# Performance work log

Measured on AMD Instinct MI355X. Metric: run time of the kernel, lower is better.

Reference implementation:

```python
import jax, jax.numpy as jnp
import numpy as np

N = 50000
E = 800000
D = 512
H = 256
K = 16
COLLAPSE_REG = 1.0


def setup_inputs() -> dict:
    key = jax.random.key(0)
    ks = jax.random.split(key, 8)
    embeddings = jax.random.normal(ks[0], (N, D), dtype=jnp.float32)
    edge_src = jax.random.randint(ks[1], (E,), 0, N, dtype=jnp.int32)
    edge_dst = jax.random.randint(ks[2], (E,), 0, N, dtype=jnp.int32)
    # GCNConv params (glorot-ish scaling)
    W1 = jax.random.normal(ks[3], (D, H), dtype=jnp.float32) / np.sqrt(D)
    b1 = jnp.zeros((H,), dtype=jnp.float32)
    W2 = jax.random.normal(ks[4], (H, H), dtype=jnp.float32) / np.sqrt(H)
    b2 = jnp.zeros((H,), dtype=jnp.float32)
    Wa = jax.random.normal(ks[5], (H, K), dtype=jnp.float32) / np.sqrt(H)
    ba = jnp.zeros((K,), dtype=jnp.float32)
    return {"embeddings": embeddings, "edge_src": edge_src, "edge_dst": edge_dst,
            "W1": W1, "b1": b1, "W2": W2, "b2": b2, "Wa": Wa, "ba": ba}


def _gcn_conv(x, W, b, src, dst, dis):
    # PyG GCNConv: transform then D^{-1/2}(A+I)D^{-1/2} aggregation + bias.
    x = x @ W                                   # [N, out]
    norm = dis[src] * dis[dst]                  # [E]
    agg = jax.ops.segment_sum(x[src] * norm[:, None], dst, num_segments=N)
    agg = agg + (dis * dis)[:, None] * x        # self-loop term
    return agg + b


def reference(embeddings, edge_src, edge_dst, W1, b1, W2, b2, Wa, ba):
    # symmetric-norm degrees with self-loops (edge weight 1)
    deg = 1.0 + jax.ops.segment_sum(jnp.ones((E,), jnp.float32), edge_dst, num_segments=N)
    dis = jax.lax.rsqrt(deg)                    # deg > 0 always (self-loop)

    x = jax.nn.selu(_gcn_conv(embeddings, W1, b1, edge_src, edge_dst, dis))
    x_skip = x  # dropout is identity in eval
    x = jax.nn.selu(_gcn_conv(x, W2, b2, edge_src, edge_dst, dis))
    x = x + x_skip
    assignments = jax.nn.softmax(x @ Wa + ba, axis=1)   # [N, K]

    # ---- DMoN losses (faithful to original, incl. scalar normalizer) ----
    degrees = jax.ops.segment_sum(jnp.ones((E,), jnp.float32), edge_src, num_segments=N)  # row sums of A
    m = degrees.sum() / 2.0
    AS = jax.ops.segment_sum(assignments[edge_dst], edge_src, num_segments=N)  # A @ S, [N, K]
    trace_pooled = jnp.sum(assignments * AS)    # trace(S^T A S)
    dS = degrees @ assignments                  # [K]
    normalizer = jnp.dot(dS, dS) / (2.0 * m)    # scalar (as in original code)
    spectral_loss = -(trace_pooled - K * normalizer) / (2.0 * m)

    cluster_sizes = assignments.sum(axis=0)     # [K]
    collapse_loss = jnp.linalg.norm(cluster_sizes) / N * jnp.sqrt(jnp.float32(K)) - 1.0
    entropy = -jnp.sum(assignments * jnp.log(assignments + 1e-8)) / N
    entropy_loss = -0.1 * entropy
    total_loss = spectral_loss + COLLAPSE_REG * collapse_loss + entropy_loss

    pooled = (assignments / (cluster_sizes + 1e-8)).T @ embeddings  # [K, D]
    return (assignments, pooled, spectral_loss, COLLAPSE_REG * collapse_loss, total_loss, entropy_loss)
```

## Files before the change

kernel.cpp:

```cpp
#include <hip/hip_runtime.h>
#include <hip/hip_fp16.h>
#include <math.h>

#define NN 50000
#define EE 800000
#define DD 512
#define HH 256
#define KK 16
#define NB_SCAN 196

typedef _Float16 half8_t __attribute__((ext_vector_type(8)));
typedef float f32x4 __attribute__((ext_vector_type(4)));

__global__ void zero_kernel(int* __restrict__ p, int n) {
    int i = blockIdx.x * blockDim.x + threadIdx.x;
    if (i < n) p[i] = 0;
}

__global__ void count_kernel(const int4* __restrict__ src4, const int4* __restrict__ dst4,
                             int* __restrict__ indeg, int* __restrict__ outdeg) {
    int e = blockIdx.x * blockDim.x + threadIdx.x;
    if (e < EE / 4) {
        int4 s = src4[e], d = dst4[e];
        atomicAdd(&outdeg[s.x], 1); atomicAdd(&outdeg[s.y], 1);
        atomicAdd(&outdeg[s.z], 1); atomicAdd(&outdeg[s.w], 1);
        atomicAdd(&indeg[d.x], 1);  atomicAdd(&indeg[d.y], 1);
        atomicAdd(&indeg[d.z], 1);  atomicAdd(&indeg[d.w], 1);
    }
}

__global__ void scan_p1(const int* __restrict__ in, int* __restrict__ part, int n,
                        const int* __restrict__ outdeg, float* __restrict__ dis,
                        float* __restrict__ degf) {
    __shared__ int tile[256];
    int t = threadIdx.x;
    int i = blockIdx.x * 256 + t;
    int v = (i < n) ? in[i] : 0;
    tile[t] = v;
    if (i < n) {
        dis[i]  = 1.0f / sqrtf(1.0f + (float)v);
        degf[i] = (float)outdeg[i];
    }
    __syncthreads();
    for (int o = 128; o > 0; o >>= 1) {
        if (t < o) tile[t] += tile[t + o];
        __syncthreads();
    }
    if (t == 0) part[blockIdx.x] = tile[0];
}

__global__ void scan_p2(int* __restrict__ part, int nb, int* __restrict__ off_end) {
    __shared__ int tile[256];
    int t = threadIdx.x;
    int v = (t < nb) ? part[t] : 0;
    tile[t] = v;
    __syncthreads();
    for (int o = 1; o < 256; o <<= 1) {
        int x = (t >= o) ? tile[t - o] : 0;
        __syncthreads();
        tile[t] += x;
        __syncthreads();
    }
    if (t < nb) part[t] = tile[t] - v;
    if (t == 255) *off_end = tile[255];
}

__global__ void scan_p3(const int* __restrict__ in, const int* __restrict__ part,
                        int* __restrict__ out, int n) {
    __shared__ int tile[256];
    int t = threadIdx.x;
    int i = blockIdx.x * 256 + t;
    int v = (i < n) ? in[i] : 0;
    tile[t] = v;
    __syncthreads();
    for (int o = 1; o < 256; o <<= 1) {
        int x = (t >= o) ? tile[t - o] : 0;
        __syncthreads();
        tile[t] += x;
        __syncthreads();
    }
    if (i < n) out[i] = part[blockIdx.x] + tile[t] - v;
}

__global__ void transpose_w(const float* __restrict__ W1, __half* __restrict__ Wt1,
                            const float* __restrict__ W2, __half* __restrict__ Wt2,
                            const float* __restrict__ Wa, __half* __restrict__ WaT) {
    int i = blockIdx.x * 256 + threadIdx.x;
    if (i < DD * HH) {
        int k = i / HH, n = i % HH;
        Wt1[(size_t)n * DD + k] = __float2half(W1[i]);
    } else if (i < DD * HH + HH * HH) {
        int j = i - DD * HH;
        int k = j / HH, n = j % HH;
        Wt2[(size_t)n * HH + k] = __float2half(W2[j]);
    } else if (i < DD * HH + HH * HH + HH * KK) {
        int j = i - DD * HH - HH * HH;
        int k = j / KK, n = j % KK;
        WaT[n * HH + k] = __float2half(Wa[j]);
    }
}

__global__ __launch_bounds__(256) void gemm1_scatter(
        const float* __restrict__ A, const __half* __restrict__ Bt,
        __half* __restrict__ C, int M,
        const int4* __restrict__ src4, const int4* __restrict__ dst4,
        const int* __restrict__ off, int* __restrict__ cur, int* __restrict__ nbr) {
    constexpr int SROW = 36;
    constexpr int EPG  = 4;
    constexpr int GPR  = 8;
    constexpr int RPP  = 32;
    constexpr int NP   = 4;
    constexpr int KI   = DD / 32;

    __shared__ float As[2][128 * SROW];

    int b = blockIdx.x;
    int t = threadIdx.x;
    if (b >= 784) {
        int e = (b - 784) * 256 + t;
        if (e < EE / 4) {
            int4 s = src4[e], d = dst4[e];
            int p;
            p = atomicAdd(&cur[d.x], 1); nbr[off[d.x] + p] = s.x;
            p = atomicAdd(&cur[d.y], 1); nbr[off[d.y] + p] = s.y;
            p = atomicAdd(&cur[d.z], 1); nbr[off[d.z] + p] = s.z;
            p = atomicAdd(&cur[d.w], 1); nbr[off[d.w] + p] = s.w;
        }
        return;
    }

    int wave = t >> 6, lane = t & 63, quad = lane >> 4, l16 = lane & 15;
    int row0 = (b >> 1) * 128, col0 = (b & 1) * 128;
    int wm = (wave & 1) * 64, wn = (wave >> 1) * 64;
    int srow = t / GPR, sg = t % GPR;

    f32x4 acc[4][4] = {};
    uint4 sreg[NP];
    uint4 bcur[4];

    const __half* brow[4];
#pragma unroll
    for (int ni = 0; ni < 4; ni++)
        brow[ni] = Bt + (size_t)(col0 + wn + ni * 16 + l16) * DD + quad * 8;

    auto gloadA = [&](int k0) {
#pragma unroll
        for (int p = 0; p < NP; p++) {
            int gr = row0 + p * RPP + srow;
            if (gr < M)
                sreg[p] = *(const uint4*)(A + (size_t)gr * DD + k0 + sg * EPG);
            else
                sreg[p] = make_uint4(0, 0, 0, 0);
        }
    };
    auto sstore = [&](int buf) {
#pragma unroll
        for (int p = 0; p < NP; p++)
            *(uint4*)&As[buf][(p * RPP + srow) * SROW + sg * EPG] = sreg[p];
    };

    gloadA(0);
#pragma unroll
    for (int ni = 0; ni < 4; ni++) bcur[ni] = *(const uint4*)(brow[ni]);
    sstore(0);
    __syncthreads();

#pragma unroll
    for (int i = 0; i < KI; i++) {
        int cur_b = i & 1;
        uint4 bnext[4];
        if (i + 1 < KI) {
            gloadA((i + 1) * 32);
#pragma unroll
            for (int ni = 0; ni < 4; ni++)
                bnext[ni] = *(const uint4*)(brow[ni] + (i + 1) * 32);
        }

        half8_t af[4];
#pragma unroll
        for (int mi = 0; mi < 4; mi++) {
            int row = wm + mi * 16 + l16;
            const float* pl = &As[cur_b][0] + row * SROW + quad * 8;
            float4 x0 = *(const float4*)pl;
            float4 x1 = *(const float4*)(pl + 4);
            half8_t h;
            h[0] = (_Float16)x0.x; h[1] = (_Float16)x0.y;
            h[2] = (_Float16)x0.z; h[3] = (_Float16)x0.w;
            h[4] = (_Float16)x1.x; h[5] = (_Float16)x1.y;
            h[6] = (_Float16)x1.z; h[7] = (_Float16)x1.w;
            af[mi] = h;
        }
#pragma unroll
        for (int mi = 0; mi < 4; mi++)
#pragma unroll
            for (int ni = 0; ni < 4; ni++)
                acc[mi][ni] = __builtin_amdgcn_mfma_f32_16x16x32_f16(
                    af[mi], *(half8_t*)&bcur[ni], acc[mi][ni], 0, 0, 0);

        if (i + 1 < KI) {
            sstore(cur_b ^ 1);
#pragma unroll
            for (int ni = 0; ni < 4; ni++) bcur[ni] = bnext[ni];
        }
        __syncthreads();
    }

#pragma unroll
    for (int mi = 0; mi < 4; mi++) {
#pragma unroll
        for (int r = 0; r < 4; r++) {
            int rr = row0 + wm + mi * 16 + quad * 4 + r;
            if (rr < M) {
#pragma unroll
                for (int ni = 0; ni < 4; ni++) {
                    C[(size_t)rr * HH + col0 + wn + ni * 16 + l16] =
                        __float2half(acc[mi][ni][r]);
                }
            }
        }
    }
}

template <typename TA, int KDIM>
__global__ __launch_bounds__(256) void mfma_gemm(const TA* __restrict__ A,
                                                 const __half* __restrict__ Bt,
                                                 __half* __restrict__ C, int M) {
    constexpr bool F32 = sizeof(TA) == 4;
    constexpr int SROW = F32 ? 36 : 40;
    constexpr int EPG  = F32 ? 4 : 8;
    constexpr int GPR  = 32 / EPG;
    constexpr int RPP  = 256 / GPR;
    constexpr int NP   = 128 / RPP;
    constexpr int KI   = KDIM / 32;

    __shared__ TA As[2][128 * SROW];

    int t = threadIdx.x;
    int wave = t >> 6, lane = t & 63, quad = lane >> 4, l16 = lane & 15;
    int row0 = blockIdx.x * 128, col0 = blockIdx.y * 128;
    int wm = (wave & 1) * 64, wn = (wave >> 1) * 64;
    int srow = t / GPR, sg = t % GPR;

    f32x4 acc[4][4] = {};
    uint4 sreg[NP];
    uint4 bcur[4];

    const __half* brow[4];
#pragma unroll
    for (int ni = 0; ni < 4; ni++)
        brow[ni] = Bt + (size_t)(col0 + wn + ni * 16 + l16) * KDIM + quad * 8;

    auto gloadA = [&](int k0) {
#pragma unroll
        for (int p = 0; p < NP; p++) {
            int gr = row0 + p * RPP + srow;
            if (gr < M)
                sreg[p] = *(const uint4*)(A + (size_t)gr * KDIM + k0 + sg * EPG);
            else
                sreg[p] = make_uint4(0, 0, 0, 0);
        }
    };
    auto sstore = [&](int buf) {
#pragma unroll
        for (int p = 0; p < NP; p++)
            *(uint4*)&As[buf][(p * RPP + srow) * SROW + sg * EPG] = sreg[p];
    };

    gloadA(0);
#pragma unroll
    for (int ni = 0; ni < 4; ni++) bcur[ni] = *(const uint4*)(brow[ni]);
    sstore(0);
    __syncthreads();

#pragma unroll
    for (int i = 0; i < KI; i++) {
        int cur = i & 1;
        uint4 bnext[4];
        if (i + 1 < KI) {
            gloadA((i + 1) * 32);
#pragma unroll
            for (int ni = 0; ni < 4; ni++)
                bnext[ni] = *(const uint4*)(brow[ni] + (i + 1) * 32);
        }

        half8_t af[4];
#pragma unroll
        for (int mi = 0; mi < 4; mi++) {
            int row = wm + mi * 16 + l16;
            if constexpr (F32) {
                const float* pl = (const float*)&As[cur][0] + row * SROW + quad * 8;
                float4 x0 = *(const float4*)pl;
                float4 x1 = *(const float4*)(pl + 4);
                half8_t h;
                h[0] = (_Float16)x0.x; h[1] = (_Float16)x0.y;
                h[2] = (_Float16)x0.z; h[3] = (_Float16)x0.w;
                h[4] = (_Float16)x1.x; h[5] = (_Float16)x1.y;
                h[6] = (_Float16)x1.z; h[7] = (_Float16)x1.w;
                af[mi] = h;
            } else {
                af[mi] = *(const half8_t*)&As[cur][row * SROW + quad * 8];
            }
        }
#pragma unroll
        for (int mi = 0; mi < 4; mi++)
#pragma unroll
            for (int ni = 0; ni < 4; ni++)
                acc[mi][ni] = __builtin_amdgcn_mfma_f32_16x16x32_f16(
                    af[mi], *(half8_t*)&bcur[ni], acc[mi][ni], 0, 0, 0);

        if (i + 1 < KI) {
            sstore(cur ^ 1);
#pragma unroll
            for (int ni = 0; ni < 4; ni++) bcur[ni] = bnext[ni];
        }
        __syncthreads();
    }

#pragma unroll
    for (int mi = 0; mi < 4; mi++) {
#pragma unroll
        for (int r = 0; r < 4; r++) {
            int rr = row0 + wm + mi * 16 + quad * 4 + r;
            if (rr < M) {
#pragma unroll
                for (int ni = 0; ni < 4; ni++) {
                    C[(size_t)rr * HH + col0 + wn + ni * 16 + l16] =
                        __float2half(acc[mi][ni][r]);
                }
            }
        }
    }
}

__device__ inline void fma8(float* acc, uint4 raw, float w) {
    const __half2* h = (const __half2*)&raw;
#pragma unroll
    for (int i = 0; i < 4; i++) {
        float2 f = __half22float2(h[i]);
        acc[2 * i]     += w * f.x;
        acc[2 * i + 1] += w * f.y;
    }
}

__global__ __launch_bounds__(256) void agg_selu(const __half* __restrict__ T,
                                                const float* __restrict__ dis,
                                                const int* __restrict__ off,
                                                const int* __restrict__ nbr,
                                                const float* __restrict__ bias,
                                                const __half* skip, __half* out) {
    int t = threadIdx.x;
    int l32 = t & 31;
    int n = blockIdx.x * 8 + (t >> 5);
    int c = l32 * 8;
    float dn = dis[n];

    float acc[8];
#pragma unroll
    for (int i = 0; i < 8; i++) acc[i] = 0.f;
    fma8(acc, *(const uint4*)(T + (size_t)n * HH + c), dn * dn);

    int s0 = off[n], s1 = off[n + 1];
    for (int base = s0; base < s1; base += 32) {
        int cnt = min(32, s1 - base);
        int sidv = 0; float sdsv = 0.f;
        if (l32 < cnt) {
            sidv = nbr[base + l32];
            sdsv = dis[sidv] * dn;
        }
        int j = 0;
        for (; j + 8 <= cnt; j += 8) {
            int a0 = __shfl(sidv, j, 32),     a1 = __shfl(sidv, j + 1, 32);
            int a2 = __shfl(sidv, j + 2, 32), a3 = __shfl(sidv, j + 3, 32);
            int a4 = __shfl(sidv, j + 4, 32), a5 = __shfl(sidv, j + 5, 32);
            int a6 = __shfl(sidv, j + 6, 32), a7 = __shfl(sidv, j + 7, 32);
            float w0 = __shfl(sdsv, j, 32),     w1 = __shfl(sdsv, j + 1, 32);
            float w2 = __shfl(sdsv, j + 2, 32), w3 = __shfl(sdsv, j + 3, 32);
            float w4 = __shfl(sdsv, j + 4, 32), w5 = __shfl(sdsv, j + 5, 32);
            float w6 = __shfl(sdsv, j + 6, 32), w7 = __shfl(sdsv, j + 7, 32);
            uint4 r0 = *(const uint4*)(T + (size_t)a0 * HH + c);
            uint4 r1 = *(const uint4*)(T + (size_t)a1 * HH + c);
            uint4 r2 = *(const uint4*)(T + (size_t)a2 * HH + c);
            uint4 r3 = *(const uint4*)(T + (size_t)a3 * HH + c);
            uint4 r4 = *(const uint4*)(T + (size_t)a4 * HH + c);
            uint4 r5 = *(const uint4*)(T + (size_t)a5 * HH + c);
            uint4 r6 = *(const uint4*)(T + (size_t)a6 * HH + c);
            uint4 r7 = *(const uint4*)(T + (size_t)a7 * HH + c);
            fma8(acc, r0, w0); fma8(acc, r1, w1);
            fma8(acc, r2, w2); fma8(acc, r3, w3);
            fma8(acc, r4, w4); fma8(acc, r5, w5);
            fma8(acc, r6, w6); fma8(acc, r7, w7);
        }
        for (; j < cnt; j++) {
            int s = __shfl(sidv, j, 32);
            float w = __shfl(sdsv, j, 32);
            fma8(acc, *(const uint4*)(T + (size_t)s * HH + c), w);
        }
    }

    const float scale = 1.0507009873554805f;
    const float alpha = 1.6732632423543772f;
    float4 b0 = *(const float4*)(bias + c);
    float4 b1 = *(const float4*)(bias + c + 4);
    float bb[8] = {b0.x, b0.y, b0.z, b0.w, b1.x, b1.y, b1.z, b1.w};
    float sk8[8];
#pragma unroll
    for (int i = 0; i < 8; i++) sk8[i] = 0.f;
    if (skip) {
        uint4 raw = *(const uint4*)(skip + (size_t)n * HH + c);
        const __half2* h = (const __half2*)&raw;
#pragma unroll
        for (int i = 0; i < 4; i++) {
            float2 f = __half22float2(h[i]);
            sk8[2 * i] = f.x; sk8[2 * i + 1] = f.y;
        }
    }
    _Float16 res[8];
#pragma unroll
    for (int i = 0; i < 8; i++) {
        float v = acc[i] + bb[i];
        float r = v > 0.f ? scale * v : scale * alpha * expm1f(v);
        res[i] = (_Float16)(r + sk8[i]);
    }
    *(uint4*)(out + (size_t)n * HH + c) = *(uint4*)res;
}

__global__ __launch_bounds__(256) void assign_mfma(const __half* __restrict__ Hb,
                                                   const __half* __restrict__ WaT,
                                                   const float* __restrict__ ba,
                                                   const float* __restrict__ degf,
                                                   float* __restrict__ out_assign,
                                                   __half* __restrict__ out_f16,
                                                   float* __restrict__ scal) {
    int t = threadIdx.x;
    int wave = t >> 6, lane = t & 63, quad = lane >> 4, l16 = lane & 15;
    int nb = blockIdx.x * 256 + wave * 64;

    f32x4 acc[4] = {};
    const __half* bp = WaT + l16 * HH + quad * 8;
    const __half* ap[4];
#pragma unroll
    for (int mi = 0; mi < 4; mi++) {
        int r = nb + mi * 16 + l16;
        if (r >= NN) r = NN - 1;
        ap[mi] = Hb + (size_t)r * HH + quad * 8;
    }
#pragma unroll
    for (int s = 0; s < 8; s++) {
        half8_t bf = *(const half8_t*)(bp + s * 32);
#pragma unroll
        for (int mi = 0; mi < 4; mi++) {
            half8_t af = *(const half8_t*)(ap[mi] + s * 32);
            acc[mi] = __builtin_amdgcn_mfma_f32_16x16x32_f16(af, bf, acc[mi], 0, 0, 0);
        }
    }

    float myb = ba[l16];
    float lcs = 0.f, ldS = 0.f, lent = 0.f;
#pragma unroll
    for (int mi = 0; mi < 4; mi++) {
#pragma unroll
        for (int r = 0; r < 4; r++) {
            int node = nb + mi * 16 + quad * 4 + r;
            bool ok = node < NN;
            float logit = acc[mi][r] + myb;
            float mx = logit;
            for (int o = 1; o < 16; o <<= 1) mx = fmaxf(mx, __shfl_xor(mx, o, 16));
            float e = expf(logit - mx);
            float sum = e;
            for (int o = 1; o < 16; o <<= 1) sum += __shfl_xor(sum, o, 16);
            float a = e / sum;
            if (ok) {
                out_assign[(size_t)node * KK + l16] = a;
                out_f16[(size_t)node * KK + l16] = __float2half(a);
                lcs += a;
                ldS += degf[node] * a;
                lent += a * logf(a + 1e-8f);
            }
        }
    }
    lcs += __shfl_xor(lcs, 16); lcs += __shfl_xor(lcs, 32);
    ldS += __shfl_xor(ldS, 16); ldS += __shfl_xor(ldS, 32);
    for (int o = 32; o >= 1; o >>= 1) lent += __shfl_xor(lent, o);
    if (quad == 0) {
        atomicAdd(&scal[l16], lcs);
        atomicAdd(&scal[16 + l16], ldS);
    }
    if (lane == 0) atomicAdd(&scal[33], lent);
}

__device__ inline float dot16h(const __half* a, const __half* b) {
    uint4 a0 = *(const uint4*)a, a1 = *(const uint4*)(a + 8);
    uint4 b0 = *(const uint4*)b, b1 = *(const uint4*)(b + 8);
    float p = 0.f;
    const __half2* xa = (const __half2*)&a0;
    const __half2* xb = (const __half2*)&b0;
#pragma unroll
    for (int i = 0; i < 4; i++) {
        float2 u = __half22float2(xa[i]), v = __half22float2(xb[i]);
        p += u.x * v.x + u.y * v.y;
    }
    xa = (const __half2*)&a1; xb = (const __half2*)&b1;
#pragma unroll
    for (int i = 0; i < 4; i++) {
        float2 u = __half22float2(xa[i]), v = __half22float2(xb[i]);
        p += u.x * v.x + u.y * v.y;
    }
    return p;
}

#define PCH 125
__global__ __launch_bounds__(256) void trace_pooled(const int4* __restrict__ src4,
                                                    const int4* __restrict__ dst4,
                                                    const __half* __restrict__ Ah,
                                                    float* __restrict__ scal,
                                                    const float* __restrict__ emb,
                                                    const float* __restrict__ assign,
                                                    float* __restrict__ part) {
    __shared__ float sa[PCH * KK];
    int bx = blockIdx.x, t = threadIdx.x;
    if (bx < 782) {
        int e = bx * 256 + t;
        float p = 0.f;
        if (e < EE / 4) {
            int4 s = src4[e], d = dst4[e];
            p += dot16h(Ah + (size_t)s.x * KK, Ah + (size_t)d.x * KK);
            p += dot16h(Ah + (size_t)s.y * KK, Ah + (size_t)d.y * KK);
            p += dot16h(Ah + (size_t)s.z * KK, Ah + (size_t)d.z * KK);
            p += dot16h(Ah + (size_t)s.w * KK, Ah + (size_t)d.w * KK);
        }
        for (int o = 32; o >= 1; o >>= 1) p += __shfl_xor(p, o);
        if (t == 0) sa[0] = 0.f;
        __syncthreads();
        if ((t & 63) == 0) atomicAdd(&sa[0], p);
        __syncthreads();
        if (t == 0) atomicAdd(&scal[32], sa[0]);
    } else {
        int j = bx - 782;
        int d = (j & 1) * 256 + t;
        int by = j >> 1;
        int c0 = by * PCH;
        float acc[KK];
#pragma unroll
        for (int k = 0; k < KK; k++) acc[k] = 0.f;
        {
            const float4* srcv = (const float4*)(assign + (size_t)c0 * KK);
            float4* dstv = (float4*)sa;
            for (int i = t; i < PCH * KK / 4; i += 256) dstv[i] = srcv[i];
        }
        __syncthreads();
        for (int jj = 0; jj < PCH; jj++) {
            float ev = emb[(size_t)(c0 + jj) * DD + d];
#pragma unroll
            for (int k4 = 0; k4 < 4; k4++) {
                float4 s4 = *(const float4*)&sa[jj * KK + k4 * 4];
                acc[k4 * 4 + 0] += s4.x * ev;
                acc[k4 * 4 + 1] += s4.y * ev;
                acc[k4 * 4 + 2] += s4.z * ev;
                acc[k4 * 4 + 3] += s4.w * ev;
            }
        }
        float* dst = part + (size_t)by * (KK * DD);
#pragma unroll
        for (int k = 0; k < KK; k++) dst[k * DD + d] = acc[k];
    }
}

__global__ void finalize(const float* __restrict__ part, const float* __restrict__ scal,
                         float* __restrict__ out) {
    int bx = blockIdx.x, t = threadIdx.x;
    if (bx < 32) {
        int i = bx * 256 + t;
        float s0 = 0.f, s1 = 0.f, s2 = 0.f, s3 = 0.f;
        for (int p = 0; p < 400; p += 4) {
            s0 += part[(size_t)p * 8192 + i];
            s1 += part[(size_t)(p + 1) * 8192 + i];
            s2 += part[(size_t)(p + 2) * 8192 + i];
            s3 += part[(size_t)(p + 3) * 8192 + i];
        }
        int k = i >> 9;
        out[800000 + i] = (s0 + s1 + s2 + s3) / (scal[k] + 1e-8f);
    } else if (t == 0) {
        float cs2 = 0.f, ds2 = 0.f;
        for (int k = 0; k < KK; k++) {
            cs2 += scal[k] * scal[k];
            ds2 += scal[16 + k] * scal[16 + k];
        }
        float two_m = (float)EE;
        float normalizer = ds2 / two_m;
        float trace = scal[32];
        float spectral = -(trace - (float)KK * normalizer) / two_m;
        float collapse = sqrtf(cs2) / (float)NN * 4.0f - 1.0f;
        float entl = 0.1f * scal[33] / (float)NN;
        out[808192] = spectral;
        out[808193] = collapse;
        out[808194] = spectral + collapse + entl;
        out[808195] = entl;
    }
}

extern "C" void kernel_launch(void* const* d_in, const int* in_sizes, int n_in,
                              void* d_out, int out_size, void* d_ws, size_t ws_size,
                              hipStream_t stream) {
    const float* emb = (const float*)d_in[0];
    const int* esrc  = (const int*)d_in[1];
    const int* edst  = (const int*)d_in[2];
    const float* W1  = (const float*)d_in[3];
    const float* b1  = (const float*)d_in[4];
    const float* W2  = (const float*)d_in[5];
    const float* b2  = (const float*)d_in[6];
    const float* Wa  = (const float*)d_in[7];
    const float* ba  = (const float*)d_in[8];
    float* out = (float*)d_out;

    int* indeg      = (int*)d_ws;
    int* outdeg     = indeg + 50000;
    int* cur        = outdeg + 50000;
    float* pool_acc = (float*)(cur + 50000);
    float* scal     = pool_acc + 8192;
    int* part       = (int*)(scal + 64);
    int* off        = part + 256;
    int* nbr        = off + 50004;
    float* dis      = (float*)(nbr + 800000);
    float* degf     = dis + 50000;
    __half* Wt1     = (__half*)(degf + 50000);
    __half* Wt2     = Wt1 + 256 * 512;
    __half* WaT     = Wt2 + 256 * 256;
    __half* T       = WaT + 16 * 256;
    __half* Hb      = T + (size_t)NN * HH;
    __half* Ah      = T;
    float* pool_part = (float*)Hb;

    zero_kernel<<<dim3(619), 256, 0, stream>>>((int*)d_ws, 158256);
    count_kernel<<<dim3(782), 256, 0, stream>>>((const int4*)esrc, (const int4*)edst,
                                                indeg, outdeg);

    scan_p1<<<dim3(NB_SCAN), 256, 0, stream>>>(indeg, part, NN, outdeg, dis, degf);
    scan_p2<<<dim3(1), 256, 0, stream>>>(part, NB_SCAN, off + NN);
    scan_p3<<<dim3(NB_SCAN), 256, 0, stream>>>(indeg, part, off, NN);

    transpose_w<<<dim3(784), 256, 0, stream>>>(W1, Wt1, W2, Wt2, Wa, WaT);

    gemm1_scatter<<<dim3(1566), 256, 0, stream>>>(emb, Wt1, T, NN,
                                                  (const int4*)esrc, (const int4*)edst,
                                                  off, cur, nbr);
    agg_selu<<<dim3(6250), 256, 0, stream>>>(T, dis, off, nbr, b1, nullptr, Hb);

    mfma_gemm<__half, HH><<<dim3(392, 2), 256, 0, stream>>>(Hb, Wt2, T, NN);
    agg_selu<<<dim3(6250), 256, 0, stream>>>(T, dis, off, nbr, b2, Hb, Hb);

    assign_mfma<<<dim3(196), 256, 0, stream>>>(Hb, WaT, ba, degf, out, Ah, scal);
    trace_pooled<<<dim3(1582), 256, 0, stream>>>((const int4*)esrc, (const int4*)edst,
                                                 Ah, scal, emb, out, pool_part);
    finalize<<<dim3(33), 256, 0, stream>>>(pool_part, scal, out);
}
```

Baseline: 576.9 us.

## Fuse second aggregation with assignment softmax and merge count with weight transpose

The second agg_selu now also computes the skip add, the Wa projection (fp32 in shared memory, via warp shuffle reduction), the softmax, and the loss partial sums, replacing the separate assign_mfma kernel and the round trip of the hidden state to memory. The count kernel absorbs the W1/W2 transpose, and zeroing becomes a hipMemsetAsync. trace_pooled reads fp32 assignments instead of an fp16 copy. The cost is that every block reloads all of Wa into shared memory, plus extra shuffle reductions, more registers per thread, and more bytes per edge in trace_pooled.

```diff
diff --git a/kernel.cpp b/kernel.cpp
--- a/kernel.cpp
+++ b/kernel.cpp
@@ -12,20 +12,30 @@
 typedef _Float16 half8_t __attribute__((ext_vector_type(8)));
 typedef float f32x4 __attribute__((ext_vector_type(4)));
 
-__global__ void zero_kernel(int* __restrict__ p, int n) {
-    int i = blockIdx.x * blockDim.x + threadIdx.x;
-    if (i < n) p[i] = 0;
-}
-
-__global__ void count_kernel(const int4* __restrict__ src4, const int4* __restrict__ dst4,
-                             int* __restrict__ indeg, int* __restrict__ outdeg) {
-    int e = blockIdx.x * blockDim.x + threadIdx.x;
-    if (e < EE / 4) {
-        int4 s = src4[e], d = dst4[e];
-        atomicAdd(&outdeg[s.x], 1); atomicAdd(&outdeg[s.y], 1);
-        atomicAdd(&outdeg[s.z], 1); atomicAdd(&outdeg[s.w], 1);
-        atomicAdd(&indeg[d.x], 1);  atomicAdd(&indeg[d.y], 1);
-        atomicAdd(&indeg[d.z], 1);  atomicAdd(&indeg[d.w], 1);
+__global__ void count_transpose(const int4* __restrict__ src4, const int4* __restrict__ dst4,
+                                int* __restrict__ indeg, int* __restrict__ outdeg,
+                                const float* __restrict__ W1, __half* __restrict__ Wt1,
+                                const float* __restrict__ W2, __half* __restrict__ Wt2) {
+    int bx = blockIdx.x;
+    if (bx < 782) {
+        int e = bx * 256 + threadIdx.x;
+        if (e < EE / 4) {
+            int4 s = src4[e], d = dst4[e];
+            atomicAdd(&outdeg[s.x], 1); atomicAdd(&outdeg[s.y], 1);
+            atomicAdd(&outdeg[s.z], 1); atomicAdd(&outdeg[s.w], 1);
+            atomicAdd(&indeg[d.x], 1);  atomicAdd(&indeg[d.y], 1);
+            atomicAdd(&indeg[d.z], 1);  atomicAdd(&indeg[d.w], 1);
+        }
+    } else {
+        int i = (bx - 782) * 256 + threadIdx.x;
+        if (i < DD * HH) {
+            int k = i / HH, n = i % HH;
+            Wt1[(size_t)n * DD + k] = __float2half(W1[i]);
+        } else if (i < DD * HH + HH * HH) {
+            int j = i - DD * HH;
+            int k = j / HH, n = j % HH;
+            Wt2[(size_t)n * HH + k] = __float2half(W2[j]);
+        }
     }
 }
 
@@ -80,24 +90,6 @@
         __syncthreads();
     }
     if (i < n) out[i] = part[blockIdx.x] + tile[t] - v;
-}
-
-__global__ void transpose_w(const float* __restrict__ W1, __half* __restrict__ Wt1,
-                            const float* __restrict__ W2, __half* __restrict__ Wt2,
-                            const float* __restrict__ Wa, __half* __restrict__ WaT) {
-    int i = blockIdx.x * 256 + threadIdx.x;
-    if (i < DD * HH) {
-        int k = i / HH, n = i % HH;
-        Wt1[(size_t)n * DD + k] = __float2half(W1[i]);
-    } else if (i < DD * HH + HH * HH) {
-        int j = i - DD * HH;
-        int k = j / HH, n = j % HH;
-        Wt2[(size_t)n * HH + k] = __float2half(W2[j]);
-    } else if (i < DD * HH + HH * HH + HH * KK) {
-        int j = i - DD * HH - HH * HH;
-        int k = j / KK, n = j % KK;
-        WaT[n * HH + k] = __float2half(Wa[j]);
-    }
 }
 
 __global__ __launch_bounds__(256) void gemm1_scatter(
@@ -342,24 +334,15 @@
     }
 }
 
-__global__ __launch_bounds__(256) void agg_selu(const __half* __restrict__ T,
-                                                const float* __restrict__ dis,
-                                                const int* __restrict__ off,
-                                                const int* __restrict__ nbr,
-                                                const float* __restrict__ bias,
-                                                const __half* skip, __half* out) {
-    int t = threadIdx.x;
-    int l32 = t & 31;
-    int n = blockIdx.x * 8 + (t >> 5);
-    int c = l32 * 8;
-    float dn = dis[n];
-
-    float acc[8];
+__device__ inline void agg_body(const __half* __restrict__ T, const float* __restrict__ dis,
+                                const int* __restrict__ off, const int* __restrict__ nbr,
+                                int n, int c, float dn, float* acc) {
 #pragma unroll
     for (int i = 0; i < 8; i++) acc[i] = 0.f;
     fma8(acc, *(const uint4*)(T + (size_t)n * HH + c), dn * dn);
 
     int s0 = off[n], s1 = off[n + 1];
+    int l32 = c >> 3;
     for (int base = s0; base < s1; base += 32) {
         int cnt = min(32, s1 - base);
         int sidv = 0; float sdsv = 0.f;
@@ -396,114 +379,135 @@
             fma8(acc, *(const uint4*)(T + (size_t)s * HH + c), w);
         }
     }
+}
+
+__global__ __launch_bounds__(256) void agg_selu(const __half* __restrict__ T,
+                                                const float* __restrict__ dis,
+                                                const int* __restrict__ off,
+                                                const int* __restrict__ nbr,
+                                                const float* __restrict__ bias,
+                                                __half* out) {
+    int t = threadIdx.x;
+    int l32 = t & 31;
+    int n = blockIdx.x * 8 + (t >> 5);
+    int c = l32 * 8;
+    float dn = dis[n];
+
+    float acc[8];
+    agg_body(T, dis, off, nbr, n, c, dn, acc);
 
     const float scale = 1.0507009873554805f;
     const float alpha = 1.6732632423543772f;
     float4 b0 = *(const float4*)(bias + c);
     float4 b1 = *(const float4*)(bias + c + 4);
     float bb[8] = {b0.x, b0.y, b0.z, b0.w, b1.x, b1.y, b1.z, b1.w};
-    float sk8[8];
-#pragma unroll
-    for (int i = 0; i < 8; i++) sk8[i] = 0.f;
-    if (skip) {
-        uint4 raw = *(const uint4*)(skip + (size_t)n * HH + c);
-        const __half2* h = (const __half2*)&raw;
-#pragma unroll
-        for (int i = 0; i < 4; i++) {
-            float2 f = __half22float2(h[i]);
-            sk8[2 * i] = f.x; sk8[2 * i + 1] = f.y;
-        }
-    }
     _Float16 res[8];
 #pragma unroll
     for (int i = 0; i < 8; i++) {
         float v = acc[i] + bb[i];
         float r = v > 0.f ? scale * v : scale * alpha * expm1f(v);
-        res[i] = (_Float16)(r + sk8[i]);
+        res[i] = (_Float16)r;
     }
     *(uint4*)(out + (size_t)n * HH + c) = *(uint4*)res;
 }
 
-__global__ __launch_bounds__(256) void assign_mfma(const __half* __restrict__ Hb,
-                                                   const __half* __restrict__ WaT,
-                                                   const float* __restrict__ ba,
-                                                   const float* __restrict__ degf,
-                                                   float* __restrict__ out_assign,
-                                                   __half* __restrict__ out_f16,
-                                                   float* __restrict__ scal) {
+__global__ __launch_bounds__(256) void agg_selu_assign(
+        const __half* __restrict__ T, const float* __restrict__ dis,
+        const int* __restrict__ off, const int* __restrict__ nbr,
+        const float* __restrict__ bias, const __half* __restrict__ skip,
+        const float* __restrict__ Wa, const float* __restrict__ ba,
+        const float* __restrict__ degf,
+        float* __restrict__ out_assign, float* __restrict__ scal) {
+    __shared__ float wa_l[8 * 16 * 32];
+    __shared__ float sba[16];
+    __shared__ float sacc[33];
+
     int t = threadIdx.x;
-    int wave = t >> 6, lane = t & 63, quad = lane >> 4, l16 = lane & 15;
-    int nb = blockIdx.x * 256 + wave * 64;
-
-    f32x4 acc[4] = {};
-    const __half* bp = WaT + l16 * HH + quad * 8;
-    const __half* ap[4];
-#pragma unroll
-    for (int mi = 0; mi < 4; mi++) {
-        int r = nb + mi * 16 + l16;
-        if (r >= NN) r = NN - 1;
-        ap[mi] = Hb + (size_t)r * HH + quad * 8;
-    }
-#pragma unroll
-    for (int s = 0; s < 8; s++) {
-        half8_t bf = *(const half8_t*)(bp + s * 32);
-#pragma unroll
-        for (int mi = 0; mi < 4; mi++) {
-            half8_t af = *(const half8_t*)(ap[mi] + s * 32);
-            acc[mi] = __builtin_amdgcn_mfma_f32_16x16x32_f16(af, bf, acc[mi], 0, 0, 0);
-        }
-    }
-
-    float myb = ba[l16];
-    float lcs = 0.f, ldS = 0.f, lent = 0.f;
-#pragma unroll
-    for (int mi = 0; mi < 4; mi++) {
-#pragma unroll
-        for (int r = 0; r < 4; r++) {
-            int node = nb + mi * 16 + quad * 4 + r;
-            bool ok = node < NN;
-            float logit = acc[mi][r] + myb;
-            float mx = logit;
-            for (int o = 1; o < 16; o <<= 1) mx = fmaxf(mx, __shfl_xor(mx, o, 16));
-            float e = expf(logit - mx);
-            float sum = e;
-            for (int o = 1; o < 16; o <<= 1) sum += __shfl_xor(sum, o, 16);
-            float a = e / sum;
-            if (ok) {
-                out_assign[(size_t)node * KK + l16] = a;
-                out_f16[(size_t)node * KK + l16] = __float2half(a);
-                lcs += a;
-                ldS += degf[node] * a;
-                lent += a * logf(a + 1e-8f);
-            }
-        }
-    }
-    lcs += __shfl_xor(lcs, 16); lcs += __shfl_xor(lcs, 32);
-    ldS += __shfl_xor(ldS, 16); ldS += __shfl_xor(ldS, 32);
-    for (int o = 32; o >= 1; o >>= 1) lent += __shfl_xor(lent, o);
-    if (quad == 0) {
-        atomicAdd(&scal[l16], lcs);
-        atomicAdd(&scal[16 + l16], ldS);
-    }
-    if (lane == 0) atomicAdd(&scal[33], lent);
-}
-
-__device__ inline float dot16h(const __half* a, const __half* b) {
-    uint4 a0 = *(const uint4*)a, a1 = *(const uint4*)(a + 8);
-    uint4 b0 = *(const uint4*)b, b1 = *(const uint4*)(b + 8);
+    int l32 = t & 31;
+    int n = blockIdx.x * 8 + (t >> 5);
+    int c = l32 * 8;
+
+    for (int idx = t; idx < 4096; idx += 256) {
+        int row = idx >> 4, k = idx & 15;
+        wa_l[((row & 7) * 16 + k) * 32 + (row >> 3)] = Wa[idx];
+    }
+    if (t < 16) sba[t] = ba[t];
+    if (t < 33) sacc[t] = 0.f;
+    __syncthreads();
+
+    float dn = dis[n];
+    float acc[8];
+    agg_body(T, dis, off, nbr, n, c, dn, acc);
+
+    const float scale = 1.0507009873554805f;
+    const float alpha = 1.6732632423543772f;
+    float4 b0 = *(const float4*)(bias + c);
+    float4 b1 = *(const float4*)(bias + c + 4);
+    float bb[8] = {b0.x, b0.y, b0.z, b0.w, b1.x, b1.y, b1.z, b1.w};
+    uint4 skraw = *(const uint4*)(skip + (size_t)n * HH + c);
+    const __half2* skh = (const __half2*)&skraw;
+
+    float hv[8];
+#pragma unroll
+    for (int i = 0; i < 8; i++) {
+        float v = acc[i] + bb[i];
+        float r = v > 0.f ? scale * v : scale * alpha * expm1f(v);
+        float2 f = __half22float2(skh[i >> 1]);
+        hv[i] = r + ((i & 1) ? f.y : f.x);
+    }
+
+    float p[16];
+#pragma unroll
+    for (int k = 0; k < 16; k++) p[k] = 0.f;
+#pragma unroll
+    for (int i = 0; i < 8; i++)
+#pragma unroll
+        for (int k = 0; k < 16; k++)
+            p[k] += hv[i] * wa_l[(i * 16 + k) * 32 + l32];
+#pragma unroll
+    for (int o = 1; o < 32; o <<= 1)
+#pragma unroll
+        for (int k = 0; k < 16; k++)
+            p[k] += __shfl_xor(p[k], o, 32);
+#pragma unroll
+    for (int k = 0; k < 16; k++) p[k] += sba[k];
+
+    float mx = p[0];
+#pragma unroll
+    for (int k = 1; k < 16; k++) mx = fmaxf(mx, p[k]);
+    float s = 0.f;
+#pragma unroll
+    for (int k = 0; k < 16; k++) { p[k] = expf(p[k] - mx); s += p[k]; }
+    float inv = 1.f / s;
+    float ent = 0.f;
+#pragma unroll
+    for (int k = 0; k < 16; k++) { p[k] *= inv; ent += p[k] * logf(p[k] + 1e-8f); }
+
+    float dgf = degf[n];
+    if (l32 == 0) {
+        float4* ov = (float4*)(out_assign + (size_t)n * KK);
+        ov[0] = make_float4(p[0], p[1], p[2], p[3]);
+        ov[1] = make_float4(p[4], p[5], p[6], p[7]);
+        ov[2] = make_float4(p[8], p[9], p[10], p[11]);
+        ov[3] = make_float4(p[12], p[13], p[14], p[15]);
+#pragma unroll
+        for (int k = 0; k < 16; k++) {
+            atomicAdd(&sacc[k], p[k]);
+            atomicAdd(&sacc[16 + k], dgf * p[k]);
+        }
+        atomicAdd(&sacc[32], ent);
+    }
+    __syncthreads();
+    if (t < 32) atomicAdd(&scal[t], sacc[t]);
+    else if (t == 32) atomicAdd(&scal[33], sacc[32]);
+}
+
+__device__ inline float dot16f(const float* a, const float* b) {
     float p = 0.f;
-    const __half2* xa = (const __half2*)&a0;
-    const __half2* xb = (const __half2*)&b0;
-#pragma unroll
-    for (int i = 0; i < 4; i++) {
-        float2 u = __half22float2(xa[i]), v = __half22float2(xb[i]);
-        p += u.x * v.x + u.y * v.y;
-    }
-    xa = (const __half2*)&a1; xb = (const __half2*)&b1;
-#pragma unroll
-    for (int i = 0; i < 4; i++) {
-        float2 u = __half22float2(xa[i]), v = __half22float2(xb[i]);
-        p += u.x * v.x + u.y * v.y;
+#pragma unroll
+    for (int q = 0; q < 4; q++) {
+        float4 u = ((const float4*)a)[q], v = ((const float4*)b)[q];
+        p += u.x * v.x + u.y * v.y + u.z * v.z + u.w * v.w;
     }
     return p;
 }
@@ -511,7 +515,6 @@
 #define PCH 125
 __global__ __launch_bounds__(256) void trace_pooled(const int4* __restrict__ src4,
                                                     const int4* __restrict__ dst4,
-                                                    const __half* __restrict__ Ah,
                                                     float* __restrict__ scal,
                                                     const float* __restrict__ emb,
                                                     const float* __restrict__ assign,
@@ -523,10 +526,10 @@
         float p = 0.f;
         if (e < EE / 4) {
             int4 s = src4[e], d = dst4[e];
-            p += dot16h(Ah + (size_t)s.x * KK, Ah + (size_t)d.x * KK);
-            p += dot16h(Ah + (size_t)s.y * KK, Ah + (size_t)d.y * KK);
-            p += dot16h(Ah + (size_t)s.z * KK, Ah + (size_t)d.z * KK);
-            p += dot16h(Ah + (size_t)s.w * KK, Ah + (size_t)d.w * KK);
+            p += dot16f(assign + (size_t)s.x * KK, assign + (size_t)d.x * KK);
+            p += dot16f(assign + (size_t)s.y * KK, assign + (size_t)d.y * KK);
+            p += dot16f(assign + (size_t)s.z * KK, assign + (size_t)d.z * KK);
+            p += dot16f(assign + (size_t)s.w * KK, assign + (size_t)d.w * KK);
         }
         for (int o = 32; o >= 1; o >>= 1) p += __shfl_xor(p, o);
         if (t == 0) sa[0] = 0.f;
@@ -627,29 +630,26 @@
     __half* WaT     = Wt2 + 256 * 256;
     __half* T       = WaT + 16 * 256;
     __half* Hb      = T + (size_t)NN * HH;
-    __half* Ah      = T;
     float* pool_part = (float*)Hb;
 
-    zero_kernel<<<dim3(619), 256, 0, stream>>>((int*)d_ws, 158256);
-    count_kernel<<<dim3(782), 256, 0, stream>>>((const int4*)esrc, (const int4*)edst,
-                                                indeg, outdeg);
+    hipMemsetAsync(d_ws, 0, 158256 * sizeof(int), stream);
+    count_transpose<<<dim3(1550), 256, 0, stream>>>((const int4*)esrc, (const int4*)edst,
+                                                    indeg, outdeg, W1, Wt1, W2, Wt2);
 
     scan_p1<<<dim3(NB_SCAN), 256, 0, stream>>>(indeg, part, NN, outdeg, dis, degf);
     scan_p2<<<dim3(1), 256, 0, stream>>>(part, NB_SCAN, off + NN);
     scan_p3<<<dim3(NB_SCAN), 256, 0, stream>>>(indeg, part, off, NN);
 
-    transpose_w<<<dim3(784), 256, 0, stream>>>(W1, Wt1, W2, Wt2, Wa, WaT);
-
     gemm1_scatter<<<dim3(1566), 256, 0, stream>>>(emb, Wt1, T, NN,
                                                   (const int4*)esrc, (const int4*)edst,
                                                   off, cur, nbr);
-    agg_selu<<<dim3(6250), 256, 0, stream>>>(T, dis, off, nbr, b1, nullptr, Hb);
+    agg_selu<<<dim3(6250), 256, 0, stream>>>(T, dis, off, nbr, b1, Hb);
 
     mfma_gemm<__half, HH><<<dim3(392, 2), 256, 0, stream>>>(Hb, Wt2, T, NN);
-    agg_selu<<<dim3(6250), 256, 0, stream>>>(T, dis, off, nbr, b2, Hb, Hb);
-
-    assign_mfma<<<dim3(196), 256, 0, stream>>>(Hb, WaT, ba, degf, out, Ah, scal);
+    agg_selu_assign<<<dim3(6250), 256, 0, stream>>>(T, dis, off, nbr, b2, Hb,
+                                                    Wa, ba, degf, out, scal);
+
     trace_pooled<<<dim3(1582), 256, 0, stream>>>((const int4*)esrc, (const int4*)edst,
-                                                 Ah, scal, emb, out, pool_part);
+                                                 scal, emb, out, pool_part);
     finalize<<<dim3(33), 256, 0, stream>>>(pool_part, scal, out);
 }
```

New measurement: 631.1 us. 9.4% more time.
